# Kernel tuning notes

Hardware: AMD Instinct MI355X
Metric: run time of the kernel (lower is better)

Reference implementation:

```python
import jax, jax.numpy as jnp
import numpy as np

ALPHA = 0.7
NUM_HEADS = 12
NUM_KV_HEADS = 6
HEAD_DIM = 64
ROPE_BASE = 10000.0


def ternary_quantize(w):
    thr = ALPHA * jnp.mean(jnp.abs(w))
    return jnp.sign(w) * (jnp.abs(w) >= thr).astype(w.dtype)


def bitlinear(x, w):
    # forward: F.linear(x, ternary(w)) * mean(|w|)
    scale = jnp.mean(jnp.abs(w))
    qw = ternary_quantize(w)
    return (x @ qw.T) * scale


def rope_tables(seq_len, dim, dtype):
    inv_freq = 1.0 / (ROPE_BASE ** (jnp.arange(0, dim, 2, dtype=jnp.float32) / dim))
    t = jnp.arange(seq_len, dtype=jnp.float32)
    freqs = jnp.outer(t, inv_freq)            # [S, dim/2]
    emb = jnp.concatenate([freqs, freqs], -1)  # [S, dim]
    return jnp.cos(emb).astype(dtype), jnp.sin(emb).astype(dtype)


def rotate_half(x):
    x1, x2 = jnp.split(x, 2, axis=-1)
    return jnp.concatenate([-x2, x1], axis=-1)


def setup_inputs() -> dict:
    key = jax.random.key(0)
    ks = jax.random.split(key, 5)
    B, S, H = 2, 2048, 768
    return {
        "hidden_states": jax.random.normal(ks[0], (B, S, H), jnp.float32),
        "Wq": jax.random.normal(ks[1], (768, 768), jnp.float32) * 0.02,
        "Wk": jax.random.normal(ks[2], (384, 768), jnp.float32) * 0.02,
        "Wv": jax.random.normal(ks[3], (384, 768), jnp.float32) * 0.02,
        "Wo": jax.random.normal(ks[4], (768, 768), jnp.float32) * 0.02,
    }


def reference(hidden_states, Wq, Wk, Wv, Wo):
    B, S, H = hidden_states.shape
    nh, nkv, hd = NUM_HEADS, NUM_KV_HEADS, HEAD_DIM
    groups = nh // nkv

    q = bitlinear(hidden_states, Wq).reshape(B, S, nh, hd).transpose(0, 2, 1, 3)
    k = bitlinear(hidden_states, Wk).reshape(B, S, nkv, hd).transpose(0, 2, 1, 3)
    v = bitlinear(hidden_states, Wv).reshape(B, S, nkv, hd).transpose(0, 2, 1, 3)

    cos, sin = rope_tables(S, hd, hidden_states.dtype)  # [S, hd]
    cos = cos[None, None]  # [1,1,S,hd]
    sin = sin[None, None]
    q = q * cos + rotate_half(q) * sin
    k = k * cos + rotate_half(k) * sin

    # GQA: expand kv heads to full head count
    k = jnp.repeat(k, groups, axis=1)  # [B, nh, S, hd]
    v = jnp.repeat(v, groups, axis=1)

    scale = 1.0 / jnp.sqrt(jnp.asarray(hd, hidden_states.dtype))
    scores = jnp.einsum("bhsd,bhtd->bhst", q, k) * scale
    attn = jax.nn.softmax(scores, axis=-1)
    out = jnp.einsum("bhst,bhtd->bhsd", attn, v)
    out = out.transpose(0, 2, 1, 3).reshape(B, S, H)
    return bitlinear(out, Wo)
```

## Files before the change

kernel.cpp:

```cpp
#include <hip/hip_runtime.h>
#include <cmath>

typedef unsigned short u16;
typedef unsigned int u32;
typedef __bf16 bf16x2 __attribute__((ext_vector_type(2)));
typedef __bf16 bf16x8 __attribute__((ext_vector_type(8)));
typedef float f32x16 __attribute__((ext_vector_type(16)));

#define NQ (768*768)
#define NK (384*768)

__device__ __forceinline__ u16 f2bf(float f) {
  u32 u = __float_as_uint(f);
  u32 r = (u + 0x7FFFu + ((u >> 16) & 1u)) >> 16;
  return (u16)r;
}
__device__ __forceinline__ u32 packbf(float a, float b) {
#if __has_builtin(__builtin_amdgcn_cvt_pk_bf16_f32)
  bf16x2 v = __builtin_amdgcn_cvt_pk_bf16_f32(a, b);
  u32 r; __builtin_memcpy(&r, &v, 4); return r;
#else
  return (u32)f2bf(a) | ((u32)f2bf(b) << 16);
#endif
}
__device__ __forceinline__ float fexp2(float x) {
#if __has_builtin(__builtin_amdgcn_exp2f)
  return __builtin_amdgcn_exp2f(x);
#else
  return exp2f(x);
#endif
}
__device__ __forceinline__ bf16x8 ldfrag(const u16* p) { bf16x8 v; __builtin_memcpy(&v, p, 16); return v; }
__device__ __forceinline__ f32x16 mfma32_(bf16x8 a, bf16x8 b, f32x16 c) {
  return __builtin_amdgcn_mfma_f32_32x32x16_bf16(a, b, c, 0, 0, 0);
}

__device__ __forceinline__ int fidx(int r, int k) {
  return (r >> 5) * 24576 + (k >> 4) * 512 + ((r & 31) + 32 * ((k >> 3) & 1)) * 8 + (k & 7);
}
__device__ __forceinline__ int kidx(int b6kvh, int s, int d) {
  return b6kvh * 131072 + (s >> 5) * 2048 + (d >> 4) * 512 +
         ((s & 31) + 32 * ((d >> 3) & 1)) * 8 + (d & 7);
}
__device__ __forceinline__ int qidx(int b, int s, int h, int d) {
  return ((b * 64 + (s >> 5)) * 12 + h) * 2048 + (d >> 4) * 512 +
         ((s & 31) + 32 * ((d >> 3) & 1)) * 8 + (d & 7);
}
__device__ __forceinline__ int vidx(int b6kvh, int d, int p) {
  return b6kvh * 131072 + (p >> 6) * 4096 + (d >> 5) * 2048 + ((p >> 4) & 3) * 512 +
         ((d & 31) + 32 * ((p >> 3) & 1)) * 8 + (p & 7);
}

__global__ __launch_bounds__(256) void abssum_kernel(const float* __restrict__ wq, const float* __restrict__ wk,
                                                     const float* __restrict__ wv, const float* __restrict__ wo,
                                                     float* __restrict__ part) {
  int which = blockIdx.y;
  const float* w = (which == 0) ? wq : (which == 1) ? wk : (which == 2) ? wv : wo;
  int n4 = ((which == 0 || which == 3) ? NQ : NK) >> 2;
  const float4* w4 = (const float4*)w;
  float s = 0.f;
  for (int i = blockIdx.x * blockDim.x + threadIdx.x; i < n4; i += gridDim.x * blockDim.x) {
    float4 v = w4[i];
    s += fabsf(v.x) + fabsf(v.y) + fabsf(v.z) + fabsf(v.w);
  }
  for (int off = 32; off; off >>= 1) s += __shfl_down(s, off);
  __shared__ float ls[4];
  if ((threadIdx.x & 63) == 0) ls[threadIdx.x >> 6] = s;
  __syncthreads();
  if (threadIdx.x == 0) part[which * 64 + blockIdx.x] = ls[0] + ls[1] + ls[2] + ls[3];
}

__global__ __launch_bounds__(256) void prep_kernel(const float* __restrict__ wq, const float* __restrict__ wk,
                                                   const float* __restrict__ wv, const float* __restrict__ wo,
                                                   const float* __restrict__ part, const float* __restrict__ x,
                                                   u16* __restrict__ qw, u16* __restrict__ woq,
                                                   u16* __restrict__ xb) {
  __shared__ float ssum[4];
  {
    int t = threadIdx.x, wv64 = t >> 6, ln = t & 63;
    float p = part[t];
    for (int off = 32; off; off >>= 1) p += __shfl_down(p, off);
    if (ln == 0) ssum[wv64] = p;
  }
  __syncthreads();
  int i = blockIdx.x * blockDim.x + threadIdx.x;
  if (i < 221184) {
    int n = i / 96, k8 = i - n * 96;
    const float* src; float th; u16* dst; int nd;
    if (n < 768)       { src = wq + n * 768;          th = 0.7f * ssum[0] * (1.f / NQ); dst = qw;  nd = n; }
    else if (n < 1152) { src = wk + (n - 768) * 768;  th = 0.7f * ssum[1] * (1.f / NK); dst = qw;  nd = n; }
    else if (n < 1536) { src = wv + (n - 1152) * 768; th = 0.7f * ssum[2] * (1.f / NK); dst = qw;  nd = n; }
    else               { src = wo + (n - 1536) * 768; th = 0.7f * ssum[3] * (1.f / NQ); dst = woq; nd = n - 1536; }
    const float4* sp = (const float4*)(src + k8 * 8);
    float4 v0 = sp[0], v1 = sp[1];
    float e[8] = {v0.x, v0.y, v0.z, v0.w, v1.x, v1.y, v1.z, v1.w};
    u16 o[8];
#pragma unroll
    for (int j = 0; j < 8; j++)
      o[j] = f2bf((fabsf(e[j]) >= th) ? ((e[j] > 0.f) ? 1.f : -1.f) : 0.f);
    __builtin_memcpy(dst + fidx(nd, k8 * 8), o, 16);
  } else {
    int j = i - 221184;
    int m = j / 96, k8 = j - m * 96;
    const float4* xp = (const float4*)(x + m * 768 + k8 * 8);
    float4 v0 = xp[0], v1 = xp[1];
    u16 o[8] = { f2bf(v0.x), f2bf(v0.y), f2bf(v0.z), f2bf(v0.w),
                 f2bf(v1.x), f2bf(v1.y), f2bf(v1.z), f2bf(v1.w) };
    __builtin_memcpy(xb + fidx(m, k8 * 8), o, 16);
  }
}

__global__ __launch_bounds__(256, 3) void gemm_qkv_kernel(const u16* __restrict__ xb, const u16* __restrict__ qw,
                                                          const float* __restrict__ part,
                                                          u16* __restrict__ qb, u16* __restrict__ kb,
                                                          u16* __restrict__ vT) {
  __shared__ float ssum[4];
  {
    int t = threadIdx.x, wv64 = t >> 6, ln = t & 63;
    float p = part[t];
    for (int off = 32; off; off >>= 1) p += __shfl_down(p, off);
    if (ln == 0) ssum[wv64] = p;
  }
  int tn = blockIdx.x, tm = blockIdx.y;
  int t = threadIdx.x, lane = t & 63, w = t >> 6, c = lane & 31, g2 = lane >> 5;
  const u16* abase = xb + (tm * 4 + w) * 24576 + lane * 8;
  const u16* bbase0 = qw + (tn * 2) * 24576 + lane * 8;
  const u16* bbase1 = bbase0 + 24576;
  f32x16 acc[2]; acc[0] = (f32x16)0.f; acc[1] = (f32x16)0.f;
  for (int kk = 0; kk < 48; kk += 4) {
#pragma unroll
    for (int ks = 0; ks < 4; ks++) {
      bf16x8 af = ldfrag(abase + (kk + ks) * 512);
      bf16x8 b0 = ldfrag(bbase0 + (kk + ks) * 512);
      bf16x8 b1 = ldfrag(bbase1 + (kk + ks) * 512);
      acc[0] = mfma32_(af, b0, acc[0]);
      acc[1] = mfma32_(af, b1, acc[1]);
    }
  }
  __syncthreads();
  float sq = ssum[0] * (1.f / NQ) * 0.180336880111120f;
  float sk = ssum[1] * (1.f / NK);
  float sv = ssum[2] * (1.f / NK);
  int mb = tm * 128 + w * 32 + 4 * g2;
  if (tn < 18) {
    float sc = (tn < 12) ? sq : sk;
    int head = (tn < 12) ? tn : (tn - 12);
    float f = fexp2((float)c * -0.41524101186092029f);
#pragma unroll
    for (int r = 0; r < 16; r++) {
      int m = mb + (r & 3) + 8 * (r >> 2);
      int bb = m >> 11, s = m & 2047;
      float sn, cs; sincosf((float)s * f, &sn, &cs);
      float x1 = acc[0][r] * sc, x2 = acc[1][r] * sc;
      u16 y1 = f2bf(x1 * cs - x2 * sn);
      u16 y2 = f2bf(x2 * cs + x1 * sn);
      if (tn < 12) {
        qb[qidx(bb, s, head, c)]      = y1;
        qb[qidx(bb, s, head, c + 32)] = y2;
      } else {
        kb[kidx(bb * 6 + head, s, c)]      = y1;
        kb[kidx(bb * 6 + head, s, c + 32)] = y2;
      }
    }
  } else {
    int kvh = tn - 18;
#pragma unroll
    for (int nb = 0; nb < 2; nb++)
#pragma unroll
      for (int r = 0; r < 16; r++) {
        int m = mb + (r & 3) + 8 * (r >> 2);
        int bb = m >> 11, s = m & 2047;
        int sp = (s & ~12) | ((s & 4) << 1) | ((s & 8) >> 1);
        vT[vidx(bb * 6 + kvh, nb * 32 + c, sp)] = f2bf(acc[nb][r] * sv);
      }
  }
}

__global__ __launch_bounds__(256, 3) void attn_kernel(const u16* __restrict__ qb, const u16* __restrict__ kb,
                                                      const u16* __restrict__ vT, u16* __restrict__ ab) {
  __shared__ float Obuf[4][32][66];
  __shared__ float Lbuf[4][32];
  int bk = blockIdx.x, qt = blockIdx.y;
  int b = bk / 6, kvh = bk % 6;
  int t = threadIdx.x, lane = t & 63, w = t >> 6, c = lane & 31, g2 = lane >> 5;
  int hn = w & 1, kh = w >> 1;

  const u16* qbase = qb + ((b * 64 + qt) * 12 + kvh * 2 + hn) * 2048;
  bf16x8 qf[4];
#pragma unroll
  for (int ks = 0; ks < 4; ks++) qf[ks] = ldfrag(qbase + ks * 512 + lane * 8);

  f32x16 fz = (f32x16)0.f;
  f32x16 O[2] = {fz, fz};
  float esum[16];
#pragma unroll
  for (int r = 0; r < 16; r++) esum[r] = 0.f;

  const u16* Kb = kb + bk * 131072;
  const u16* Vb = vT + bk * 131072;

#pragma unroll 2
  for (int it = 0; it < 32; it++) {
    int kb32 = kh * 32 + it;
    const u16* kt = Kb + kb32 * 2048;
    const u16* vt = Vb + (kb32 >> 1) * 4096 + (kb32 & 1) * 1024;
    bf16x8 kf[4];
#pragma unroll
    for (int ks = 0; ks < 4; ks++) kf[ks] = ldfrag(kt + ks * 512 + lane * 8);
    bf16x8 vf[2][2];
#pragma unroll
    for (int dn = 0; dn < 2; dn++)
#pragma unroll
      for (int ksv = 0; ksv < 2; ksv++)
        vf[dn][ksv] = ldfrag(vt + dn * 2048 + ksv * 512 + lane * 8);
    f32x16 S0 = fz, S1 = fz;
    S0 = mfma32_(kf[0], qf[0], S0);
    S1 = mfma32_(kf[1], qf[1], S1);
    S0 = mfma32_(kf[2], qf[2], S0);
    S1 = mfma32_(kf[3], qf[3], S1);
    float e[16];
#pragma unroll
    for (int r = 0; r < 16; r++) {
      e[r] = fexp2(S0[r] + S1[r]);
      esum[r] += e[r];
    }
    u32 P[8];
#pragma unroll
    for (int j = 0; j < 8; j++) P[j] = packbf(e[2 * j], e[2 * j + 1]);
    bf16x8 PA[2];
    __builtin_memcpy(&PA[0], &P[0], 16);
    __builtin_memcpy(&PA[1], &P[4], 16);
#pragma unroll
    for (int ksv = 0; ksv < 2; ksv++) {
      O[0] = mfma32_(PA[ksv], vf[0][ksv], O[0]);
      O[1] = mfma32_(PA[ksv], vf[1][ksv], O[1]);
    }
  }
#pragma unroll
  for (int r = 0; r < 16; r++) {
    float v = esum[r];
    v += __shfl_xor(v, 1); v += __shfl_xor(v, 2); v += __shfl_xor(v, 4);
    v += __shfl_xor(v, 8); v += __shfl_xor(v, 16);
    esum[r] = v;
  }
  if (c == 0) {
#pragma unroll
    for (int r = 0; r < 16; r++) Lbuf[w][(r & 3) + 8 * (r >> 2) + 4 * g2] = esum[r];
  }
#pragma unroll
  for (int dn = 0; dn < 2; dn++)
#pragma unroll
    for (int r = 0; r < 16; r++)
      Obuf[w][(r & 3) + 8 * (r >> 2) + 4 * g2][dn * 32 + c] = O[dn][r];
  __syncthreads();
  {
    int hn_c = t >> 7, qq = (t >> 2) & 31, dc = (t & 3) * 16;
    float l = Lbuf[hn_c][qq] + Lbuf[hn_c + 2][qq];
    float inv = 1.f / l;
    u16 o[16];
#pragma unroll
    for (int j = 0; j < 16; j++)
      o[j] = f2bf((Obuf[hn_c][qq][dc + j] + Obuf[hn_c + 2][qq][dc + j]) * inv);
    int h = kvh * 2 + hn_c;
    int mg = b * 64 + qt;
    u16* dst = ab + mg * 24576 + ((h * 64 + dc) >> 4) * 512 + qq * 8;
    __builtin_memcpy(dst, o, 16);
    __builtin_memcpy(dst + 256, o + 8, 16);
  }
}

__global__ __launch_bounds__(256, 3) void gemm_out_kernel(const u16* __restrict__ ab, const u16* __restrict__ woq,
                                                          const float* __restrict__ part, float* __restrict__ out) {
  __shared__ float ssum4;
  {
    int t = threadIdx.x;
    if (t < 64) {
      float p = part[192 + t];
      for (int off = 32; off; off >>= 1) p += __shfl_down(p, off);
      if (t == 0) ssum4 = p;
    }
  }
  int tn = blockIdx.x, tm = blockIdx.y;
  int t = threadIdx.x, lane = t & 63, w = t >> 6, c = lane & 31, g2 = lane >> 5;
  const u16* abase = ab + (tm * 4 + w) * 24576 + lane * 8;
  const u16* bbase0 = woq + (tn * 2) * 24576 + lane * 8;
  const u16* bbase1 = bbase0 + 24576;
  f32x16 acc[2]; acc[0] = (f32x16)0.f; acc[1] = (f32x16)0.f;
  for (int kk = 0; kk < 48; kk += 4) {
#pragma unroll
    for (int ks = 0; ks < 4; ks++) {
      bf16x8 af = ldfrag(abase + (kk + ks) * 512);
      bf16x8 b0 = ldfrag(bbase0 + (kk + ks) * 512);
      bf16x8 b1 = ldfrag(bbase1 + (kk + ks) * 512);
      acc[0] = mfma32_(af, b0, acc[0]);
      acc[1] = mfma32_(af, b1, acc[1]);
    }
  }
  __syncthreads();
  float so = ssum4 * (1.f / NQ);
  int mb = tm * 128 + w * 32 + 4 * g2;
#pragma unroll
  for (int nb = 0; nb < 2; nb++)
#pragma unroll
    for (int r = 0; r < 16; r++) {
      int m = mb + (r & 3) + 8 * (r >> 2);
      out[m * 768 + tn * 64 + nb * 32 + c] = acc[nb][r] * so;
    }
}

extern "C" void kernel_launch(void* const* d_in, const int* in_sizes, int n_in,
                              void* d_out, int out_size, void* d_ws, size_t ws_size,
                              hipStream_t stream) {
  const float* x  = (const float*)d_in[0];
  const float* wq = (const float*)d_in[1];
  const float* wk = (const float*)d_in[2];
  const float* wv = (const float*)d_in[3];
  const float* wo = (const float*)d_in[4];
  float* out = (float*)d_out;
  char* ws = (char*)d_ws;

  u16* qw  = (u16*)(ws + 256);
  u16* woq = (u16*)(ws + 2359552);
  u16* xb  = (u16*)(ws + 3539200);
  u16* qb  = (u16*)(ws + 9830656);
  u16* kb  = (u16*)(ws + 16122112);
  u16* vT  = (u16*)(ws + 19267840);
  u16* ab  = (u16*)(ws + 22413568);
  float* part = (float*)(ws + 28705024);

  dim3 blk(256);
  abssum_kernel<<<dim3(64, 4), blk, 0, stream>>>(wq, wk, wv, wo, part);
  prep_kernel<<<dim3(2400), blk, 0, stream>>>(wq, wk, wv, wo, part, x, qw, woq, xb);
  gemm_qkv_kernel<<<dim3(24, 32), blk, 0, stream>>>(xb, qw, part, qb, kb, vT);
  attn_kernel<<<dim3(12, 64), blk, 0, stream>>>(qb, kb, vT, ab);
  gemm_out_kernel<<<dim3(12, 32), blk, 0, stream>>>(ab, woq, part, out);
}
```

Baseline: 167.4 us.

## Retile GEMM warps to 2x2 layout and compute softmax row sums with MFMA

The QKV and output GEMMs now give each block a 64-row tile with its four waves arranged 2x2 over M and N, instead of four waves stacked along M. The output GEMM drops to one 32x32 tile per wave and launches twice as many blocks. In attention, the exp row sums are no longer accumulated per lane and reduced with shuffles; an extra MFMA against a vector of ones accumulates them alongside the P·V product. The QK score MFMAs now use a single accumulator chain, and the unroll-2 pragma on the attention loop is removed. This is meant to improve GEMM occupancy and operand reuse and to cut VALU and shuffle work, at the cost of a serial MFMA dependency chain and extra MFMA issue per iteration.

```diff
diff --git a/kernel.cpp b/kernel.cpp
--- a/kernel.cpp
+++ b/kernel.cpp
@@ -123,8 +123,9 @@
   }
   int tn = blockIdx.x, tm = blockIdx.y;
   int t = threadIdx.x, lane = t & 63, w = t >> 6, c = lane & 31, g2 = lane >> 5;
-  const u16* abase = xb + (tm * 4 + w) * 24576 + lane * 8;
-  const u16* bbase0 = qw + (tn * 2) * 24576 + lane * 8;
+  int wm = w & 1, wn = w >> 1;
+  const u16* abase = xb + (tm * 2 + wm) * 24576 + lane * 8;
+  const u16* bbase0 = qw + (tn * 4 + wn * 2) * 24576 + lane * 8;
   const u16* bbase1 = bbase0 + 24576;
   f32x16 acc[2]; acc[0] = (f32x16)0.f; acc[1] = (f32x16)0.f;
   for (int kk = 0; kk < 48; kk += 4) {
@@ -141,10 +142,10 @@
   float sq = ssum[0] * (1.f / NQ) * 0.180336880111120f;
   float sk = ssum[1] * (1.f / NK);
   float sv = ssum[2] * (1.f / NK);
-  int mb = tm * 128 + w * 32 + 4 * g2;
-  if (tn < 18) {
-    float sc = (tn < 12) ? sq : sk;
-    int head = (tn < 12) ? tn : (tn - 12);
+  int mb = tm * 64 + wm * 32 + 4 * g2;
+  if (tn < 9) {
+    float sc = (tn < 6) ? sq : sk;
+    int head = (tn < 6) ? (tn * 2 + wn) : ((tn - 6) * 2 + wn);
     float f = fexp2((float)c * -0.41524101186092029f);
 #pragma unroll
     for (int r = 0; r < 16; r++) {
@@ -154,7 +155,7 @@
       float x1 = acc[0][r] * sc, x2 = acc[1][r] * sc;
       u16 y1 = f2bf(x1 * cs - x2 * sn);
       u16 y2 = f2bf(x2 * cs + x1 * sn);
-      if (tn < 12) {
+      if (tn < 6) {
         qb[qidx(bb, s, head, c)]      = y1;
         qb[qidx(bb, s, head, c + 32)] = y2;
       } else {
@@ -163,7 +164,7 @@
       }
     }
   } else {
-    int kvh = tn - 18;
+    int kvh = (tn - 9) * 2 + wn;
 #pragma unroll
     for (int nb = 0; nb < 2; nb++)
 #pragma unroll
@@ -190,16 +191,17 @@
 #pragma unroll
   for (int ks = 0; ks < 4; ks++) qf[ks] = ldfrag(qbase + ks * 512 + lane * 8);
 
+  u32 onesw = 0x3F803F80u;
+  bf16x8 ones;
+  { u32 tmp[4] = {onesw, onesw, onesw, onesw}; __builtin_memcpy(&ones, tmp, 16); }
+
   f32x16 fz = (f32x16)0.f;
   f32x16 O[2] = {fz, fz};
-  float esum[16];
-#pragma unroll
-  for (int r = 0; r < 16; r++) esum[r] = 0.f;
+  f32x16 Lacc = fz;
 
   const u16* Kb = kb + bk * 131072;
   const u16* Vb = vT + bk * 131072;
 
-#pragma unroll 2
   for (int it = 0; it < 32; it++) {
     int kb32 = kh * 32 + it;
     const u16* kt = Kb + kb32 * 2048;
@@ -213,17 +215,12 @@
 #pragma unroll
       for (int ksv = 0; ksv < 2; ksv++)
         vf[dn][ksv] = ldfrag(vt + dn * 2048 + ksv * 512 + lane * 8);
-    f32x16 S0 = fz, S1 = fz;
-    S0 = mfma32_(kf[0], qf[0], S0);
-    S1 = mfma32_(kf[1], qf[1], S1);
-    S0 = mfma32_(kf[2], qf[2], S0);
-    S1 = mfma32_(kf[3], qf[3], S1);
+    f32x16 S = fz;
+#pragma unroll
+    for (int ks = 0; ks < 4; ks++) S = mfma32_(kf[ks], qf[ks], S);
     float e[16];
 #pragma unroll
-    for (int r = 0; r < 16; r++) {
-      e[r] = fexp2(S0[r] + S1[r]);
-      esum[r] += e[r];
-    }
+    for (int r = 0; r < 16; r++) e[r] = fexp2(S[r]);
     u32 P[8];
 #pragma unroll
     for (int j = 0; j < 8; j++) P[j] = packbf(e[2 * j], e[2 * j + 1]);
@@ -234,18 +231,12 @@
     for (int ksv = 0; ksv < 2; ksv++) {
       O[0] = mfma32_(PA[ksv], vf[0][ksv], O[0]);
       O[1] = mfma32_(PA[ksv], vf[1][ksv], O[1]);
-    }
-  }
-#pragma unroll
-  for (int r = 0; r < 16; r++) {
-    float v = esum[r];
-    v += __shfl_xor(v, 1); v += __shfl_xor(v, 2); v += __shfl_xor(v, 4);
-    v += __shfl_xor(v, 8); v += __shfl_xor(v, 16);
-    esum[r] = v;
+      Lacc = mfma32_(PA[ksv], ones, Lacc);
+    }
   }
   if (c == 0) {
 #pragma unroll
-    for (int r = 0; r < 16; r++) Lbuf[w][(r & 3) + 8 * (r >> 2) + 4 * g2] = esum[r];
+    for (int r = 0; r < 16; r++) Lbuf[w][(r & 3) + 8 * (r >> 2) + 4 * g2] = Lacc[r];
   }
 #pragma unroll
   for (int dn = 0; dn < 2; dn++)
@@ -282,30 +273,26 @@
   }
   int tn = blockIdx.x, tm = blockIdx.y;
   int t = threadIdx.x, lane = t & 63, w = t >> 6, c = lane & 31, g2 = lane >> 5;
-  const u16* abase = ab + (tm * 4 + w) * 24576 + lane * 8;
-  const u16* bbase0 = woq + (tn * 2) * 24576 + lane * 8;
-  const u16* bbase1 = bbase0 + 24576;
-  f32x16 acc[2]; acc[0] = (f32x16)0.f; acc[1] = (f32x16)0.f;
+  int wm = w & 1, wn = w >> 1;
+  const u16* abase = ab + (tm * 2 + wm) * 24576 + lane * 8;
+  const u16* bbase = woq + (tn * 2 + wn) * 24576 + lane * 8;
+  f32x16 acc = (f32x16)0.f;
   for (int kk = 0; kk < 48; kk += 4) {
 #pragma unroll
     for (int ks = 0; ks < 4; ks++) {
       bf16x8 af = ldfrag(abase + (kk + ks) * 512);
-      bf16x8 b0 = ldfrag(bbase0 + (kk + ks) * 512);
-      bf16x8 b1 = ldfrag(bbase1 + (kk + ks) * 512);
-      acc[0] = mfma32_(af, b0, acc[0]);
-      acc[1] = mfma32_(af, b1, acc[1]);
+      bf16x8 bf = ldfrag(bbase + (kk + ks) * 512);
+      acc = mfma32_(af, bf, acc);
     }
   }
   __syncthreads();
   float so = ssum4 * (1.f / NQ);
-  int mb = tm * 128 + w * 32 + 4 * g2;
-#pragma unroll
-  for (int nb = 0; nb < 2; nb++)
-#pragma unroll
-    for (int r = 0; r < 16; r++) {
-      int m = mb + (r & 3) + 8 * (r >> 2);
-      out[m * 768 + tn * 64 + nb * 32 + c] = acc[nb][r] * so;
-    }
+  int mb = tm * 64 + wm * 32 + 4 * g2;
+#pragma unroll
+  for (int r = 0; r < 16; r++) {
+    int m = mb + (r & 3) + 8 * (r >> 2);
+    out[m * 768 + tn * 64 + wn * 32 + c] = acc[r] * so;
+  }
 }
 
 extern "C" void kernel_launch(void* const* d_in, const int* in_sizes, int n_in,
@@ -331,7 +318,7 @@
   dim3 blk(256);
   abssum_kernel<<<dim3(64, 4), blk, 0, stream>>>(wq, wk, wv, wo, part);
   prep_kernel<<<dim3(2400), blk, 0, stream>>>(wq, wk, wv, wo, part, x, qw, woq, xb);
-  gemm_qkv_kernel<<<dim3(24, 32), blk, 0, stream>>>(xb, qw, part, qb, kb, vT);
+  gemm_qkv_kernel<<<dim3(12, 64), blk, 0, stream>>>(xb, qw, part, qb, kb, vT);
   attn_kernel<<<dim3(12, 64), blk, 0, stream>>>(qb, kb, vT, ab);
-  gemm_out_kernel<<<dim3(12, 32), blk, 0, stream>>>(ab, woq, part, out);
-}
+  gemm_out_kernel<<<dim3(12, 64), blk, 0, stream>>>(ab, woq, part, out);
+}
```

New measurement: 157.7 us. 1.06x faster.
